# Kernel optimization log

Measured on AMD Instinct MI355X. Metric: run time of the kernel, lower is better.

Reference implementation:

```python
import jax, jax.numpy as jnp
import numpy as np

B = 256
M = (32, 32, 32)          # size_in modes
N = (32, 32, 32)          # size_out modes
R = (1, 16, 16, 1)        # TT ranks
CORE_SCALE = 0.05


def setup_inputs() -> dict:
    key = jax.random.key(0)
    kx, k0, k1, k2, kb = jax.random.split(key, 5)
    x = jax.random.normal(kx, (B,) + M, dtype=jnp.float32)
    # TT cores: core_i has shape [r_i, n_i, m_i, r_{i+1}]
    core0 = jax.random.normal(k0, (R[0], N[0], M[0], R[1]), dtype=jnp.float32) * CORE_SCALE
    core1 = jax.random.normal(k1, (R[1], N[1], M[1], R[2]), dtype=jnp.float32) * CORE_SCALE
    core2 = jax.random.normal(k2, (R[2], N[2], M[2], R[3]), dtype=jnp.float32) * CORE_SCALE
    bias = jax.random.normal(kb, N, dtype=jnp.float32) * 0.01
    return {"x": x, "core0": core0, "core1": core1, "core2": core2, "bias": bias}


def _tt_matvec(x, cores):
    # y[..., n1..nd] = sum_{m1..md} prod_i core_i[r_i, n_i, m_i, r_{i+1}] * x[..., m1..md]
    d = len(cores)
    batch_shape = x.shape[:-d]
    # z: [B, r, P, m_i, m_{i+1}, ..., m_d]  (P = flattened already-produced n dims)
    z = x.reshape((-1, 1, 1) + x.shape[-d:])
    n_dims = []
    for core in cores:
        r, n, m, s = core.shape
        # contract current input mode m and left rank r; append output mode n
        z = jnp.einsum('rnms,brpm...->bspn...', core, z)
        n_dims.append(n)
        sh = z.shape
        z = z.reshape(sh[:2] + (sh[2] * sh[3],) + sh[4:])  # merge P and n
    return z.reshape(batch_shape + tuple(n_dims))


def reference(x, core0, core1, core2, bias):
    y = _tt_matvec(x, (core0, core1, core2))
    return y + bias
```

## Files before the change

### kernel.cpp

```cpp
#include <hip/hip_runtime.h>


typedef __attribute__((ext_vector_type(8))) short bf16x8;
typedef __attribute__((ext_vector_type(4))) float f32x4;

#define WS_A1   0
#define WS_A0T  262144
#define WS_W2T  278528
#define WS_XT   294912
#define WS_XT_ELEMS 8388608
#define WS_NEED_BYTES ((size_t)(WS_XT + WS_XT_ELEMS) * 2)

__device__ __forceinline__ unsigned short f2bf(float f) {
    union { float f; unsigned int u; } v; v.f = f;
    unsigned int u = v.u;
    u += 0x7fffu + ((u >> 16) & 1u);
    return (unsigned short)(u >> 16);
}

template<bool XT>
__global__ void tt_prep(const float* __restrict__ x,
                        const float* __restrict__ core0,
                        const float* __restrict__ core1,
                        const float* __restrict__ core2,
                        unsigned short* __restrict__ ws)
{
    const int t = threadIdx.x;
    if (XT && blockIdx.x < 8192) {
        __shared__ float tile[32 * 36];
        const int b  = blockIdx.x >> 5;
        const int m2 = blockIdx.x & 31;
        {
            const int m1 = t >> 3, c4 = (t & 7) * 4;
            float4 v = *(const float4*)(x + (size_t)b * 32768 + m1 * 1024 + m2 * 32 + c4);
            *(float4*)&tile[m1 * 36 + c4] = v;
        }
        __syncthreads();
        {
            const int m3 = t >> 3, g = t & 7;
            unsigned short o[4];
            #pragma unroll
            for (int j = 0; j < 4; ++j)
                o[j] = f2bf(tile[(g * 4 + j) * 36 + m3]);
            unsigned short* dst = ws + WS_XT + (size_t)b * 32768 + (m2 * 32 + m3) * 32 + g * 4;
            *(uint2*)dst = *(uint2*)o;
        }
        return;
    }
    const int u = (blockIdx.x - (XT ? 8192 : 0)) * 256 + t;
    unsigned short* A1  = ws + WS_A1;
    unsigned short* A0T = ws + WS_A0T;
    unsigned short* W2T = ws + WS_W2T;
    bf16x8 o;
    if (u < 32768) {
        int e = u * 8;
        int row = e >> 9, col0 = e & 511;
        int n2 = row >> 4, s = row & 15;
        int m2 = col0 >> 4, r0 = col0 & 15;
        const float* src = core1 + n2 * 512 + m2 * 16 + s;
        #pragma unroll
        for (int j = 0; j < 8; ++j) o[j] = (short)f2bf(src[(r0 + j) * 16384]);
        *(bf16x8*)(A1 + e) = o;
    } else if (u < 34816) {
        int e = (u - 32768) * 8;
        int row = e >> 5, m1b = e & 31;
        int n1 = row >> 4, s = row & 15;
        const float* src = core0 + n1 * 512 + m1b * 16 + s;
        #pragma unroll
        for (int j = 0; j < 8; ++j) o[j] = (short)f2bf(src[j * 16]);
        *(bf16x8*)(A0T + e) = o;
    } else if (u < 36864) {
        int e = (u - 34816) * 8;
        int n3 = e >> 9, k20 = e & 511;
        int m3 = k20 >> 4, s0 = k20 & 15;
        const float* src = core2 + n3 * 32 + m3;
        #pragma unroll
        for (int j = 0; j < 8; ++j) o[j] = (short)f2bf(src[(s0 + j) * 1024]);
        *(bf16x8*)(W2T + e) = o;
    }
}

template<bool XT>
__global__ __launch_bounds__(512, 2)
void tt_mfma(const float* __restrict__ x,
             const unsigned short* __restrict__ ws,
             const float* __restrict__ bias,
             float* __restrict__ out)
{
    extern __shared__ char smem[];

    const unsigned short* A1  = ws + WS_A1;
    const unsigned short* A0T = ws + WS_A0T;
    const unsigned short* W2T = ws + WS_W2T;
    const unsigned short* xT  = ws + WS_XT;

    const int t   = threadIdx.x;
    const int l   = t & 63;
    const int w   = t >> 6;
    const int l15 = l & 15;
    const int lg  = l >> 4;

    const int bq = blockIdx.x >> 5;
    const int n1 = blockIdx.x & 31;

    {
        const int lb = w >> 1, ph = w & 1;
        const int b  = bq * 4 + lb;
        char* zb = smem + lb * 32768;
        bf16x8 afrag = *(const bf16x8*)(A0T + n1 * 512 + l15 * 32 + lg * 8);
        if (XT) {
            const unsigned short* xb = xT + (size_t)b * 32768 + lg * 8;
            #pragma unroll 4
            for (int pti = 0; pti < 32; ++pti) {
                int p = ph * 512 + pti * 16 + l15;
                bf16x8 bfrag = *(const bf16x8*)(xb + p * 32);
                f32x4 c = __builtin_amdgcn_mfma_f32_16x16x32_bf16(
                    afrag, bfrag, (f32x4){0.f, 0.f, 0.f, 0.f}, 0, 0, 0);
                int m2 = p >> 5, m3 = p & 31;
                unsigned short h[4];
                #pragma unroll
                for (int i = 0; i < 4; ++i) h[i] = f2bf(c[i]);
                int off = (m3 << 10) + (((m2 * 32 + lg * 8)) ^ ((m3 & 7) << 4));
                *(uint2*)(zb + off) = *(uint2*)h;
            }
        } else {
            const float* xb = x + (size_t)b * 32768 + (lg * 8) * 1024;
            for (int pti = 0; pti < 32; ++pti) {
                int p = ph * 512 + pti * 16 + l15;
                bf16x8 bfrag;
                #pragma unroll
                for (int j = 0; j < 8; ++j) bfrag[j] = (short)f2bf(xb[j * 1024 + p]);
                f32x4 c = __builtin_amdgcn_mfma_f32_16x16x32_bf16(
                    afrag, bfrag, (f32x4){0.f, 0.f, 0.f, 0.f}, 0, 0, 0);
                int m2 = p >> 5, m3 = p & 31;
                unsigned short h[4];
                #pragma unroll
                for (int i = 0; i < 4; ++i) h[i] = f2bf(c[i]);
                int off = (m3 << 10) + (((m2 * 32 + lg * 8)) ^ ((m3 & 7) << 4));
                *(uint2*)(zb + off) = *(uint2*)h;
            }
        }
    }
    __syncthreads();

    f32x4 acc[4][8];
    #pragma unroll
    for (int mt = 0; mt < 4; ++mt)
        #pragma unroll
        for (int nt = 0; nt < 8; ++nt)
            acc[mt][nt] = (f32x4){0.f, 0.f, 0.f, 0.f};
    {
        const unsigned short* a1p = A1 + (w * 64 + l15) * 512 + lg * 8;
        const int rsw = ((l15 & 7) << 4);
        #pragma unroll 2
        for (int ks = 0; ks < 16; ++ks) {
            int kb = ks * 64 + lg * 16;
            bf16x8 af[4];
            #pragma unroll
            for (int mt = 0; mt < 4; ++mt)
                af[mt] = *(const bf16x8*)(a1p + mt * 8192 + ks * 32);
            bf16x8 bf[8];
            #pragma unroll
            for (int b4 = 0; b4 < 4; ++b4) {
                char* zb = smem + b4 * 32768;
                int r0 = l15, r1 = 16 + l15;
                bf[b4 * 2 + 0] = *(const bf16x8*)(zb + (r0 << 10) + (kb ^ rsw));
                bf[b4 * 2 + 1] = *(const bf16x8*)(zb + (r1 << 10) + (kb ^ rsw));
            }
            #pragma unroll
            for (int mt = 0; mt < 4; ++mt)
                #pragma unroll
                for (int nt = 0; nt < 8; ++nt)
                    acc[mt][nt] = __builtin_amdgcn_mfma_f32_16x16x32_bf16(
                        af[mt], bf[nt], acc[mt][nt], 0, 0, 0);
        }
    }
    __syncthreads();

    {
        #pragma unroll
        for (int mt = 0; mt < 4; ++mt) {
            int n2 = w * 4 + mt;
            int rowbase = n2 << 10;
            int swz = (n2 & 7) << 4;
            #pragma unroll
            for (int nt = 0; nt < 8; ++nt) {
                char* zb = smem + (nt >> 1) * 32768;
                int m3 = (nt & 1) * 16 + l15;
                unsigned short h[4];
                #pragma unroll
                for (int i = 0; i < 4; ++i) h[i] = f2bf(acc[mt][nt][i]);
                int off = rowbase + ((m3 * 32 + lg * 8) ^ swz);
                *(uint2*)(zb + off) = *(uint2*)h;
            }
        }
    }
    __syncthreads();

    {
        const int lb = w >> 1, n3h = w & 1;
        const int b  = bq * 4 + lb;
        char* zb = smem + lb * 32768;
        f32x4 c[2];
        c[0] = (f32x4){0.f, 0.f, 0.f, 0.f};
        c[1] = (f32x4){0.f, 0.f, 0.f, 0.f};
        const unsigned short* w2p = W2T + (n3h * 16 + l15) * 512 + lg * 8;
        #pragma unroll 2
        for (int ks = 0; ks < 16; ++ks) {
            bf16x8 bfg = *(const bf16x8*)(w2p + ks * 32);
            #pragma unroll
            for (int mt = 0; mt < 2; ++mt) {
                int row = mt * 16 + l15;
                bf16x8 af = *(const bf16x8*)(zb + (row << 10) +
                                             ((ks * 64 + lg * 16) ^ ((row & 7) << 4)));
                c[mt] = __builtin_amdgcn_mfma_f32_16x16x32_bf16(af, bfg, c[mt], 0, 0, 0);
            }
        }
        int n3 = n3h * 16 + l15;
        size_t ob = (size_t)b * 32768 + (size_t)n1 * 1024;
        const float* bp2 = bias + n1 * 1024;
        #pragma unroll
        for (int mt = 0; mt < 2; ++mt)
            #pragma unroll
            for (int i = 0; i < 4; ++i) {
                int n2 = mt * 16 + lg * 4 + i;
                out[ob + n2 * 32 + n3] = c[mt][i] + bp2[n2 * 32 + n3];
            }
    }
}

extern "C" void kernel_launch(void* const* d_in, const int* in_sizes, int n_in,
                              void* d_out, int out_size, void* d_ws, size_t ws_size,
                              hipStream_t stream) {
    (void)in_sizes; (void)n_in; (void)out_size;
    const float* x     = (const float*)d_in[0];
    const float* core0 = (const float*)d_in[1];
    const float* core1 = (const float*)d_in[2];
    const float* core2 = (const float*)d_in[3];
    const float* bias  = (const float*)d_in[4];
    float* out = (float*)d_out;
    unsigned short* ws = (unsigned short*)d_ws;

    const int lds_bytes = 4 * 32768;
    if (ws_size >= WS_NEED_BYTES) {
        hipFuncSetAttribute((const void*)tt_mfma<true>,
                            hipFuncAttributeMaxDynamicSharedMemorySize, lds_bytes);
        tt_prep<true><<<8336, 256, 0, stream>>>(x, core0, core1, core2, ws);
        tt_mfma<true><<<2048, 512, lds_bytes, stream>>>(x, ws, bias, out);
    } else {
        hipFuncSetAttribute((const void*)tt_mfma<false>,
                            hipFuncAttributeMaxDynamicSharedMemorySize, lds_bytes);
        tt_prep<false><<<144, 256, 0, stream>>>(x, core0, core1, core2, ws);
        tt_mfma<false><<<2048, 512, lds_bytes, stream>>>(x, ws, bias, out);
    }
}
```

Before: 221.9 us.

## Software-pipeline fragment loads and swizzle block order across XCDs

Adds register double-buffering of the global and LDS fragment loads in all three MFMA stages, so the next k-step's operands are fetched while the current MFMAs issue, and fully unrolls those loops. It also remaps blockIdx so consecutive blocks on the same XCD share batch groups, aiming for better L2 reuse of x and A1. The extra buffered fragments raise register pressure and may lower occupancy or cause spills.

```diff
diff --git a/kernel.cpp b/kernel.cpp
--- a/kernel.cpp
+++ b/kernel.cpp
@@ -100,8 +100,9 @@
     const int l15 = l & 15;
     const int lg  = l >> 4;
 
-    const int bq = blockIdx.x >> 5;
-    const int n1 = blockIdx.x & 31;
+    const int swzid = (blockIdx.x & 7) * 256 + (blockIdx.x >> 3);
+    const int bq = swzid >> 5;
+    const int n1 = swzid & 31;
 
     {
         const int lb = w >> 1, ph = w & 1;
@@ -110,12 +111,17 @@
         bf16x8 afrag = *(const bf16x8*)(A0T + n1 * 512 + l15 * 32 + lg * 8);
         if (XT) {
             const unsigned short* xb = xT + (size_t)b * 32768 + lg * 8;
-            #pragma unroll 4
+            bf16x8 bfrag[2];
+            bfrag[0] = *(const bf16x8*)(xb + (ph * 512 + l15) * 32);
+            #pragma unroll
             for (int pti = 0; pti < 32; ++pti) {
+                if (pti < 31) {
+                    int pn = ph * 512 + (pti + 1) * 16 + l15;
+                    bfrag[(pti + 1) & 1] = *(const bf16x8*)(xb + pn * 32);
+                }
                 int p = ph * 512 + pti * 16 + l15;
-                bf16x8 bfrag = *(const bf16x8*)(xb + p * 32);
                 f32x4 c = __builtin_amdgcn_mfma_f32_16x16x32_bf16(
-                    afrag, bfrag, (f32x4){0.f, 0.f, 0.f, 0.f}, 0, 0, 0);
+                    afrag, bfrag[pti & 1], (f32x4){0.f, 0.f, 0.f, 0.f}, 0, 0, 0);
                 int m2 = p >> 5, m3 = p & 31;
                 unsigned short h[4];
                 #pragma unroll
@@ -152,27 +158,43 @@
     {
         const unsigned short* a1p = A1 + (w * 64 + l15) * 512 + lg * 8;
         const int rsw = ((l15 & 7) << 4);
-        #pragma unroll 2
-        for (int ks = 0; ks < 16; ++ks) {
-            int kb = ks * 64 + lg * 16;
-            bf16x8 af[4];
-            #pragma unroll
-            for (int mt = 0; mt < 4; ++mt)
-                af[mt] = *(const bf16x8*)(a1p + mt * 8192 + ks * 32);
-            bf16x8 bf[8];
+        const int rlo = l15 << 10, rhi = (16 + l15) << 10;
+
+        bf16x8 af[2][4], bf[2][8];
+        #pragma unroll
+        for (int mt = 0; mt < 4; ++mt)
+            af[0][mt] = *(const bf16x8*)(a1p + mt * 8192);
+        {
+            int kofs = (lg * 16) ^ rsw;
             #pragma unroll
             for (int b4 = 0; b4 < 4; ++b4) {
                 char* zb = smem + b4 * 32768;
-                int r0 = l15, r1 = 16 + l15;
-                bf[b4 * 2 + 0] = *(const bf16x8*)(zb + (r0 << 10) + (kb ^ rsw));
-                bf[b4 * 2 + 1] = *(const bf16x8*)(zb + (r1 << 10) + (kb ^ rsw));
+                bf[0][b4 * 2 + 0] = *(const bf16x8*)(zb + rlo + kofs);
+                bf[0][b4 * 2 + 1] = *(const bf16x8*)(zb + rhi + kofs);
+            }
+        }
+        #pragma unroll
+        for (int ks = 0; ks < 16; ++ks) {
+            const int cur = ks & 1, nxt = cur ^ 1;
+            if (ks < 15) {
+                int kb = (ks + 1) * 64 + lg * 16;
+                int kofs = kb ^ rsw;
+                #pragma unroll
+                for (int mt = 0; mt < 4; ++mt)
+                    af[nxt][mt] = *(const bf16x8*)(a1p + mt * 8192 + (ks + 1) * 32);
+                #pragma unroll
+                for (int b4 = 0; b4 < 4; ++b4) {
+                    char* zb = smem + b4 * 32768;
+                    bf[nxt][b4 * 2 + 0] = *(const bf16x8*)(zb + rlo + kofs);
+                    bf[nxt][b4 * 2 + 1] = *(const bf16x8*)(zb + rhi + kofs);
+                }
             }
             #pragma unroll
             for (int mt = 0; mt < 4; ++mt)
                 #pragma unroll
                 for (int nt = 0; nt < 8; ++nt)
                     acc[mt][nt] = __builtin_amdgcn_mfma_f32_16x16x32_bf16(
-                        af[mt], bf[nt], acc[mt][nt], 0, 0, 0);
+                        af[cur][mt], bf[cur][nt], acc[mt][nt], 0, 0, 0);
         }
     }
     __syncthreads();
@@ -205,15 +227,17 @@
         c[0] = (f32x4){0.f, 0.f, 0.f, 0.f};
         c[1] = (f32x4){0.f, 0.f, 0.f, 0.f};
         const unsigned short* w2p = W2T + (n3h * 16 + l15) * 512 + lg * 8;
-        #pragma unroll 2
+        bf16x8 bfg[2];
+        bfg[0] = *(const bf16x8*)(w2p);
+        #pragma unroll
         for (int ks = 0; ks < 16; ++ks) {
-            bf16x8 bfg = *(const bf16x8*)(w2p + ks * 32);
+            if (ks < 15) bfg[(ks + 1) & 1] = *(const bf16x8*)(w2p + (ks + 1) * 32);
             #pragma unroll
             for (int mt = 0; mt < 2; ++mt) {
                 int row = mt * 16 + l15;
                 bf16x8 af = *(const bf16x8*)(zb + (row << 10) +
                                              ((ks * 64 + lg * 16) ^ ((row & 7) << 4)));
-                c[mt] = __builtin_amdgcn_mfma_f32_16x16x32_bf16(af, bfg, c[mt], 0, 0, 0);
+                c[mt] = __builtin_amdgcn_mfma_f32_16x16x32_bf16(af, bfg[ks & 1], c[mt], 0, 0, 0);
             }
         }
         int n3 = n3h * 16 + l15;
```

New measurement: 221.7 us. About the same (-0.1%).
